# Kernel optimization log

Hardware: AMD Instinct MI355X
Metric: run time of the kernel (lower is better)

## Reference

```python
import jax, jax.numpy as jnp
import numpy as np

N, E, IN_C, HID, OUT_C, L = 100000, 1600000, 128, 128, 128, 3
BN_EPS = 1e-5


def setup_inputs() -> dict:
    key = jax.random.key(0)
    ks = jax.random.split(key, 16)
    inp = {
        "x": jax.random.normal(ks[0], (N, IN_C), dtype=jnp.float32),
        "edge_index": jax.random.randint(ks[1], (2, E), 0, N, dtype=jnp.int64),
        "edge_attr": jax.random.normal(ks[2], (E, 1), dtype=jnp.float32),
        # input/output projections (math uses [in, out] layout)
        "lin0_w": jax.random.normal(ks[3], (IN_C, HID), dtype=jnp.float32) / np.sqrt(IN_C),
        "lin0_b": jnp.zeros((HID,), dtype=jnp.float32),
        "lin1_w": jax.random.normal(ks[4], (HID, OUT_C), dtype=jnp.float32) / np.sqrt(HID),
        "lin1_b": jnp.zeros((OUT_C,), dtype=jnp.float32),
        # stacked GCNConv weights/biases
        "conv_w": jax.random.normal(ks[5], (L, HID, HID), dtype=jnp.float32) / np.sqrt(HID),
        "conv_b": jnp.zeros((L, HID), dtype=jnp.float32),
        # BatchNorm1d (eval mode: running stats are buffers)
        "bn_gamma": jnp.ones((L, HID), dtype=jnp.float32),
        "bn_beta": jnp.zeros((L, HID), dtype=jnp.float32),
        "bn_mean": 0.1 * jax.random.normal(ks[6], (L, HID), dtype=jnp.float32),
        "bn_var": jax.random.uniform(ks[7], (L, HID), minval=0.5, maxval=1.5, dtype=jnp.float32),
    }
    return inp


def reference(x, edge_index, edge_attr, lin0_w, lin0_b, lin1_w, lin1_b,
              conv_w, conv_b, bn_gamma, bn_beta, bn_mean, bn_var):
    n = x.shape[0]
    # GCN normalization with self-loops (computed once; identical every layer)
    loops = jnp.arange(n, dtype=edge_index.dtype)
    src = jnp.concatenate([edge_index[0], loops])  # [E+N]
    dst = jnp.concatenate([edge_index[1], loops])  # [E+N]
    deg = jax.ops.segment_sum(jnp.ones_like(src, dtype=x.dtype), dst, num_segments=n)
    dinv = jnp.where(deg > 0, deg ** -0.5, 0.0)
    norm = dinv[src] * dinv[dst]  # [E+N]

    # input projection + relu (dropout p used in eval -> identity)
    h = jax.nn.relu(x @ lin0_w + lin0_b)

    for l in range(L):
        hw = h @ conv_w[l]                                         # [N, H]
        msg = hw[src] * norm[:, None]                              # [E+N, H]
        agg = jax.ops.segment_sum(msg, dst, num_segments=n) + conv_b[l]
        # BatchNorm1d (inference) + ReLU activation
        h = (agg - bn_mean[l]) * jax.lax.rsqrt(bn_var[l] + BN_EPS) * bn_gamma[l] + bn_beta[l]
        h = jax.nn.relu(h)

    out = h @ lin1_w + lin1_b
    return out
```

## Files before the change

### kernel.cpp

```cpp
#include <hip/hip_runtime.h>
#include <hip/hip_fp16.h>


#define HIDC 128
#define BN_EPS 1e-5f
#define DPB 256
#define NBK 512
#define BIN_CHUNK 8192

typedef short bf16x8 __attribute__((ext_vector_type(8)));
typedef float f32x4 __attribute__((ext_vector_type(4)));

__device__ __forceinline__ unsigned short f2bf_rn(float x) {
    unsigned int u = __float_as_uint(x);
    unsigned int r = u + 0x7fffu + ((u >> 16) & 1u);
    return (unsigned short)(r >> 16);
}
__device__ __forceinline__ float bf2f(unsigned short b) {
    return __uint_as_float(((unsigned int)b) << 16);
}


__global__ void detect64(const unsigned int* ei, int* flag) {
    if (threadIdx.x != 0 || blockIdx.x != 0) return;
    int is64 = 1;
    for (int i = 0; i < 64; ++i) {
        if (ei[2 * i + 1] != 0u) { is64 = 0; break; }
    }
    *flag = is64;
}

__global__ __launch_bounds__(256) void bucket_count(const void* __restrict__ ei,
                                                    const int* __restrict__ flag,
                                                    int* __restrict__ bkt, int e) {
    __shared__ int h[NBK];
    int t = threadIdx.x;
    for (int i = t; i < NBK; i += 256) h[i] = 0;
    __syncthreads();
    int base = blockIdx.x * BIN_CHUNK;
    int cnt = e - base;
    if (cnt > BIN_CHUNK) cnt = BIN_CHUNK;
    if (*flag) {
        const long long* pd = (const long long*)ei + e;
        for (int i = t; i < cnt; i += 256) atomicAdd(&h[((int)pd[base + i]) >> 8], 1);
    } else {
        const int* pd = (const int*)ei + e;
        for (int i = t; i < cnt; i += 256) atomicAdd(&h[pd[base + i] >> 8], 1);
    }
    __syncthreads();
    for (int i = t; i < NBK; i += 256) if (h[i]) atomicAdd(&bkt[i], h[i]);
}

__global__ void scan_buckets(const int* __restrict__ bkt, int* __restrict__ bbase,
                             int* __restrict__ bc, int* __restrict__ rowptr,
                             int n, int e, int nbk) {
    __shared__ int s[NBK];
    int t = threadIdx.x;
    int v = (t < nbk) ? bkt[t] : 0;
    s[t] = v;
    __syncthreads();
    for (int off = 1; off < NBK; off <<= 1) {
        int val = (t >= off) ? s[t - off] : 0;
        __syncthreads();
        s[t] += val;
        __syncthreads();
    }
    int excl = s[t] - v;
    bbase[t] = excl;
    bc[t] = excl;
    if (t == 0) rowptr[n] = e;
}

__global__ __launch_bounds__(256) void bin_pairs(const void* __restrict__ ei,
                                                 const int* __restrict__ flag,
                                                 int* __restrict__ bc,
                                                 int2* __restrict__ staged, int e) {
    __shared__ int hist[NBK];
    __shared__ int lstart[NBK];
    __shared__ int gbase[NBK];
    __shared__ int sdata[256];
    __shared__ int2 stage[BIN_CHUNK];

    int t = threadIdx.x;
    int base = blockIdx.x * BIN_CHUNK;
    int cnt = e - base;
    if (cnt > BIN_CHUNK) cnt = BIN_CHUNK;
    int is64 = *flag;

    for (int i = t; i < NBK; i += 256) hist[i] = 0;
    __syncthreads();
    if (is64) {
        const long long* pd = (const long long*)ei + e;
        for (int i = t; i < cnt; i += 256) atomicAdd(&hist[((int)pd[base + i]) >> 8], 1);
    } else {
        const int* pd = (const int*)ei + e;
        for (int i = t; i < cnt; i += 256) atomicAdd(&hist[pd[base + i] >> 8], 1);
    }
    __syncthreads();

    int a0 = hist[2 * t], a1 = hist[2 * t + 1];
    int s = a0 + a1;
    sdata[t] = s;
    __syncthreads();
    for (int off = 1; off < 256; off <<= 1) {
        int val = (t >= off) ? sdata[t - off] : 0;
        __syncthreads();
        sdata[t] += val;
        __syncthreads();
    }
    int excl = sdata[t] - s;
    lstart[2 * t] = excl;
    lstart[2 * t + 1] = excl + a0;
    if (a0 > 0) gbase[2 * t] = atomicAdd(&bc[2 * t], a0);
    if (a1 > 0) gbase[2 * t + 1] = atomicAdd(&bc[2 * t + 1], a1);
    hist[2 * t] = excl;
    hist[2 * t + 1] = excl + a0;
    __syncthreads();

    if (is64) {
        const long long* ps = (const long long*)ei;
        const long long* pd = ps + e;
        for (int i = t; i < cnt; i += 256) {
            int2 p = make_int2((int)ps[base + i], (int)pd[base + i]);
            int pos = atomicAdd(&hist[p.y >> 8], 1);
            stage[pos] = p;
        }
    } else {
        const int* ps = (const int*)ei;
        const int* pd = ps + e;
        for (int i = t; i < cnt; i += 256) {
            int2 p = make_int2(ps[base + i], pd[base + i]);
            int pos = atomicAdd(&hist[p.y >> 8], 1);
            stage[pos] = p;
        }
    }
    __syncthreads();

    for (int i = t; i < cnt; i += 256) {
        int2 p = stage[i];
        int b = p.y >> 8;
        staged[gbase[b] + (i - lstart[b])] = p;
    }
}

__global__ __launch_bounds__(256) void fill_bucket(const int2* __restrict__ staged,
                                                   const int* __restrict__ bbase,
                                                   float* __restrict__ dinv,
                                                   int* __restrict__ rowptr,
                                                   int* __restrict__ col, int n) {
    __shared__ int cnt[DPB];
    __shared__ int scn[DPB];
    int b = blockIdx.x;
    int t = threadIdx.x;
    int dstart = b * DPB;
    int ebeg = bbase[b], eend = bbase[b + 1];
    cnt[t] = 0;
    __syncthreads();
    for (int i = ebeg + t; i < eend; i += 256)
        atomicAdd(&cnt[staged[i].y - dstart], 1);
    __syncthreads();
    int my = cnt[t];
    scn[t] = my;
    __syncthreads();
    for (int off = 1; off < 256; off <<= 1) {
        int val = (t >= off) ? scn[t - off] : 0;
        __syncthreads();
        scn[t] += val;
        __syncthreads();
    }
    int excl = scn[t] - my;
    int v = dstart + t;
    if (v < n) {
        rowptr[v] = ebeg + excl;
        dinv[v] = rsqrtf((float)(my + 1));
    }
    cnt[t] = excl;
    __syncthreads();
    for (int i = ebeg + t; i < eend; i += 256) {
        int2 p = staged[i];
        int pos = atomicAdd(&cnt[p.y - dstart], 1);
        col[ebeg + pos] = p.x;
    }
}


__global__ __launch_bounds__(256) void pack_w(const float* __restrict__ lin0,
                                              const float* __restrict__ conv,
                                              const float* __restrict__ lin1,
                                              uint4* __restrict__ wf) {
    int tid = blockIdx.x * 256 + threadIdx.x;
    if (tid >= 5 * 2048) return;
    int mat = tid >> 11;
    int rem = tid & 2047;
    int ks = rem >> 9;
    int tt = (rem >> 6) & 7;
    int l = rem & 63;
    const float* W = (mat == 0) ? lin0 : (mat == 4) ? lin1 : conv + (size_t)(mat - 1) * 16384;
    int kbase = ks * 32 + (l >> 4) * 8;
    int c = tt * 16 + (l & 15);
    unsigned int hi[4], lo[4];
#pragma unroll
    for (int d = 0; d < 4; ++d) {
        float w0 = W[(kbase + 2 * d) * 128 + c];
        float w1 = W[(kbase + 2 * d + 1) * 128 + c];
        unsigned short h0 = f2bf_rn(w0), h1 = f2bf_rn(w1);
        unsigned short l0 = f2bf_rn(w0 - bf2f(h0)), l1 = f2bf_rn(w1 - bf2f(h1));
        hi[d] = (unsigned int)h0 | ((unsigned int)h1 << 16);
        lo[d] = (unsigned int)l0 | ((unsigned int)l1 << 16);
    }
    int rec = (ks * 8 + tt) * 64 + l;
    wf[(size_t)mat * 4096 + rec] = make_uint4(hi[0], hi[1], hi[2], hi[3]);
    wf[(size_t)mat * 4096 + 2048 + rec] = make_uint4(lo[0], lo[1], lo[2], lo[3]);
}


template <int AFP16>
__global__ __launch_bounds__(512) void gemm_mfma(
    const void* __restrict__ A, const uint4* __restrict__ wf,
    const float* __restrict__ bias, const float* __restrict__ dinv,
    void* __restrict__ Cout, int M, int mode) {
    __shared__ uint4 WfL[4096];

    int t = threadIdx.x;
#pragma unroll
    for (int i = 0; i < 8; ++i) WfL[t + i * 512] = wf[t + i * 512];

    int wave = t >> 6, lane = t & 63;
    int lrow = lane & 15, lgrp = lane >> 4;
    int r0 = blockIdx.x * 128 + wave * 16;

    f32x4 acc[8];
#pragma unroll
    for (int i = 0; i < 8; ++i) acc[i] = (f32x4){0.f, 0.f, 0.f, 0.f};

    __syncthreads();

    int arow = r0 + lrow;
    if (arow >= M) arow = M - 1;
    const char* ap = (const char*)A +
        (AFP16 ? ((size_t)arow * 256 + lgrp * 16) : ((size_t)arow * 512 + lgrp * 32));

#pragma unroll
    for (int ks = 0; ks < 4; ++ks) {
        float av[8];
        if (AFP16) {
            uint4 q = *(const uint4*)(ap + ks * 64);
            unsigned int w[4] = {q.x, q.y, q.z, q.w};
#pragma unroll
            for (int d = 0; d < 4; ++d) {
                __half2 h2 = *(__half2*)&w[d];
                float2 f2 = __half22float2(h2);
                av[2 * d] = f2.x;
                av[2 * d + 1] = f2.y;
            }
        } else {
            float4 v0 = *(const float4*)(ap + ks * 128);
            float4 v1 = *(const float4*)(ap + ks * 128 + 16);
            av[0] = v0.x; av[1] = v0.y; av[2] = v0.z; av[3] = v0.w;
            av[4] = v1.x; av[5] = v1.y; av[6] = v1.z; av[7] = v1.w;
        }
        bf16x8 ahi, alo;
#pragma unroll
        for (int j = 0; j < 8; ++j) {
            unsigned short h = f2bf_rn(av[j]);
            ahi[j] = (short)h;
            alo[j] = (short)f2bf_rn(av[j] - bf2f(h));
        }
#pragma unroll
        for (int tt = 0; tt < 8; ++tt) {
            bf16x8 bhi = *(const bf16x8*)&WfL[(ks * 8 + tt) * 64 + lane];
            bf16x8 blo = *(const bf16x8*)&WfL[2048 + (ks * 8 + tt) * 64 + lane];
            acc[tt] = __builtin_amdgcn_mfma_f32_16x16x32_bf16(ahi, bhi, acc[tt], 0, 0, 0);
            acc[tt] = __builtin_amdgcn_mfma_f32_16x16x32_bf16(ahi, blo, acc[tt], 0, 0, 0);
            acc[tt] = __builtin_amdgcn_mfma_f32_16x16x32_bf16(alo, bhi, acc[tt], 0, 0, 0);
        }
    }

    int rbase = r0 + lgrp * 4;
    float dv[4] = {0.f, 0.f, 0.f, 0.f};
    if (mode == 1) {
#pragma unroll
        for (int j = 0; j < 4; ++j) dv[j] = (rbase + j < M) ? dinv[rbase + j] : 0.f;
    }
#pragma unroll
    for (int tt = 0; tt < 8; ++tt) {
        int c = tt * 16 + lrow;
        float bc_ = (mode != 1) ? bias[c] : 0.f;
#pragma unroll
        for (int j = 0; j < 4; ++j) {
            int r = rbase + j;
            if (r >= M) continue;
            float val = acc[tt][j];
            if (mode == 0) {
                ((__half*)Cout)[(size_t)r * 128 + c] = __float2half(fmaxf(val + bc_, 0.f));
            } else if (mode == 1) {
                ((__half*)Cout)[(size_t)r * 128 + c] = __float2half(val * dv[j]);
            } else {
                ((float*)Cout)[(size_t)r * 128 + c] = val + bc_;
            }
        }
    }
}


__global__ __launch_bounds__(256) void agg_bn_relu(
    const __half2* __restrict__ hw, const int* __restrict__ rowptr,
    const int* __restrict__ col, const float* __restrict__ dinv,
    const float* __restrict__ convb, const float* __restrict__ gamma,
    const float* __restrict__ beta, const float* __restrict__ mean,
    const float* __restrict__ var, __half2* __restrict__ hout, int n) {
    int lane = threadIdx.x & 63;
    int v = (blockIdx.x * 256 + threadIdx.x) >> 6;
    if (v >= n) return;

    float2 acc = __half22float2(hw[(size_t)v * 64 + lane]);

    int beg = rowptr[v], end = rowptr[v + 1];
    for (int p = beg; p < end; p += 64) {
        int cnt = end - p;
        if (cnt > 64) cnt = 64;
        int myc = (lane < cnt) ? col[p + lane] : 0;
        int j = 0;
        for (; j + 8 <= cnt; j += 8) {
            int u0 = __shfl(myc, j);
            int u1 = __shfl(myc, j + 1);
            int u2 = __shfl(myc, j + 2);
            int u3 = __shfl(myc, j + 3);
            int u4 = __shfl(myc, j + 4);
            int u5 = __shfl(myc, j + 5);
            int u6 = __shfl(myc, j + 6);
            int u7 = __shfl(myc, j + 7);
            float2 m0 = __half22float2(hw[(size_t)u0 * 64 + lane]);
            float2 m1 = __half22float2(hw[(size_t)u1 * 64 + lane]);
            float2 m2 = __half22float2(hw[(size_t)u2 * 64 + lane]);
            float2 m3 = __half22float2(hw[(size_t)u3 * 64 + lane]);
            float2 m4 = __half22float2(hw[(size_t)u4 * 64 + lane]);
            float2 m5 = __half22float2(hw[(size_t)u5 * 64 + lane]);
            float2 m6 = __half22float2(hw[(size_t)u6 * 64 + lane]);
            float2 m7 = __half22float2(hw[(size_t)u7 * 64 + lane]);
            acc.x += ((m0.x + m1.x) + (m2.x + m3.x)) + ((m4.x + m5.x) + (m6.x + m7.x));
            acc.y += ((m0.y + m1.y) + (m2.y + m3.y)) + ((m4.y + m5.y) + (m6.y + m7.y));
        }
        for (; j < cnt; ++j) {
            int u = __shfl(myc, j);
            float2 m = __half22float2(hw[(size_t)u * 64 + lane]);
            acc.x += m.x;
            acc.y += m.y;
        }
    }

    float dvv = dinv[v];
    int c0 = lane * 2;
    float2 g  = *(const float2*)(gamma + c0);
    float2 be = *(const float2*)(beta + c0);
    float2 mn = *(const float2*)(mean + c0);
    float2 va = *(const float2*)(var + c0);
    float2 cb = *(const float2*)(convb + c0);
    float s0 = g.x * rsqrtf(va.x + BN_EPS);
    float s1 = g.y * rsqrtf(va.y + BN_EPS);
    float o0 = (dvv * acc.x + cb.x - mn.x) * s0 + be.x;
    float o1 = (dvv * acc.y + cb.y - mn.y) * s1 + be.y;
    o0 = fmaxf(o0, 0.0f);
    o1 = fmaxf(o1, 0.0f);
    hout[(size_t)v * 64 + lane] = __floats2half2_rn(o0, o1);
}


extern "C" void kernel_launch(void* const* d_in, const int* in_sizes, int n_in,
                              void* d_out, int out_size, void* d_ws, size_t ws_size,
                              hipStream_t stream) {
    const float* x      = (const float*)d_in[0];
    const void*  ei     = d_in[1];
    const float* lin0_w = (const float*)d_in[3];
    const float* lin0_b = (const float*)d_in[4];
    const float* lin1_w = (const float*)d_in[5];
    const float* lin1_b = (const float*)d_in[6];
    const float* conv_w = (const float*)d_in[7];
    const float* conv_b = (const float*)d_in[8];
    const float* bn_g   = (const float*)d_in[9];
    const float* bn_b   = (const float*)d_in[10];
    const float* bn_m   = (const float*)d_in[11];
    const float* bn_v   = (const float*)d_in[12];

    int n = in_sizes[0] / HIDC;
    int e = in_sizes[1] / 2;
    int nbk = (n + DPB - 1) / DPB;

    char* ws = (char*)d_ws;
    size_t off = 0;
    auto alloc = [&](size_t bytes) -> void* {
        void* p = ws + off;
        off += (bytes + 255) & ~(size_t)255;
        return p;
    };
    __half2* h16    = (__half2*)alloc((size_t)n * HIDC * 2);
    __half2* hw     = (__half2*)alloc((size_t)n * HIDC * 2);
    int2*    staged = (int2*)alloc((size_t)e * 8);
    int*     col    = (int*)alloc((size_t)e * 4);
    float*   dinv   = (float*)alloc((size_t)n * 4);
    int*     rowptr = (int*)alloc(((size_t)n + 1) * 4);
    int*     bkt    = (int*)alloc((size_t)NBK * 4);
    int*     bbase  = (int*)alloc((size_t)(NBK + 1) * 4);
    int*     bc     = (int*)alloc((size_t)NBK * 4);
    uint4*   wf     = (uint4*)alloc((size_t)5 * 4096 * 16);
    int*     flag   = (int*)alloc(256);

    hipMemsetAsync(bkt, 0, (size_t)NBK * 4, stream);

    detect64<<<1, 64, 0, stream>>>((const unsigned int*)ei, flag);
    pack_w<<<40, 256, 0, stream>>>(lin0_w, conv_w, lin1_w, wf);

    int binb = (e + BIN_CHUNK - 1) / BIN_CHUNK;
    bucket_count<<<binb, 256, 0, stream>>>(ei, flag, bkt, e);
    scan_buckets<<<1, 512, 0, stream>>>(bkt, bbase, bc, rowptr, n, e, nbk);
    bin_pairs<<<binb, 256, 0, stream>>>(ei, flag, bc, staged, e);
    fill_bucket<<<nbk, 256, 0, stream>>>(staged, bbase, dinv, rowptr, col, n);

    int gb = (n + 127) / 128;
    gemm_mfma<0><<<gb, 512, 0, stream>>>(x, wf, lin0_b, nullptr, h16, n, 0);

    int ab = (n + 3) / 4;
    for (int l = 0; l < 3; ++l) {
        gemm_mfma<1><<<gb, 512, 0, stream>>>(h16, wf + (size_t)(1 + l) * 4096, nullptr, dinv, hw, n, 1);
        agg_bn_relu<<<ab, 256, 0, stream>>>(hw, rowptr, col, dinv,
                                            conv_b + (size_t)l * HIDC,
                                            bn_g + (size_t)l * HIDC, bn_b + (size_t)l * HIDC,
                                            bn_m + (size_t)l * HIDC, bn_v + (size_t)l * HIDC,
                                            h16, n);
    }
    gemm_mfma<1><<<gb, 512, 0, stream>>>(h16, wf + (size_t)4 * 4096, lin1_b, nullptr, d_out, n, 2);
}
```

Before: 382.7 us.

## Switch split-precision GEMM to fp16 MFMA and pack staged edge pairs into one int

The split-precision GEMM now uses fp16 MFMA instead of bf16. When the A input is already fp16 it is loaded straight into the operand with no conversion, and the low-part product is skipped, so those layers issue two MFMAs per tile instead of three. Edge staging packs the source index and the local destination offset into one 32-bit int, which halves the staged buffer traffic during CSR construction. The packing assumes node indices fit in 17 bits (N=100000 does). The fp16 hi/lo split has a narrower exponent range than bf16, so very large or very small weights or activations could lose accuracy.

```diff
diff --git a/kernel.cpp b/kernel.cpp
--- a/kernel.cpp
+++ b/kernel.cpp
@@ -8,17 +8,8 @@
 #define NBK 512
 #define BIN_CHUNK 8192
 
-typedef short bf16x8 __attribute__((ext_vector_type(8)));
+typedef _Float16 f16x8 __attribute__((ext_vector_type(8)));
 typedef float f32x4 __attribute__((ext_vector_type(4)));
-
-__device__ __forceinline__ unsigned short f2bf_rn(float x) {
-    unsigned int u = __float_as_uint(x);
-    unsigned int r = u + 0x7fffu + ((u >> 16) & 1u);
-    return (unsigned short)(r >> 16);
-}
-__device__ __forceinline__ float bf2f(unsigned short b) {
-    return __uint_as_float(((unsigned int)b) << 16);
-}
 
 
 __global__ void detect64(const unsigned int* ei, int* flag) {
@@ -74,7 +65,7 @@
 __global__ __launch_bounds__(256) void bin_pairs(const void* __restrict__ ei,
                                                  const int* __restrict__ flag,
                                                  int* __restrict__ bc,
-                                                 int2* __restrict__ staged, int e) {
+                                                 int* __restrict__ staged, int e) {
     __shared__ int hist[NBK];
     __shared__ int lstart[NBK];
     __shared__ int gbase[NBK];
@@ -139,11 +130,12 @@
     for (int i = t; i < cnt; i += 256) {
         int2 p = stage[i];
         int b = p.y >> 8;
-        staged[gbase[b] + (i - lstart[b])] = p;
-    }
-}
-
-__global__ __launch_bounds__(256) void fill_bucket(const int2* __restrict__ staged,
+        int packed = p.x | ((p.y & 255) << 17);
+        staged[gbase[b] + (i - lstart[b])] = packed;
+    }
+}
+
+__global__ __launch_bounds__(256) void fill_bucket(const int* __restrict__ staged,
                                                    const int* __restrict__ bbase,
                                                    float* __restrict__ dinv,
                                                    int* __restrict__ rowptr,
@@ -157,7 +149,7 @@
     cnt[t] = 0;
     __syncthreads();
     for (int i = ebeg + t; i < eend; i += 256)
-        atomicAdd(&cnt[staged[i].y - dstart], 1);
+        atomicAdd(&cnt[staged[i] >> 17], 1);
     __syncthreads();
     int my = cnt[t];
     scn[t] = my;
@@ -177,9 +169,9 @@
     cnt[t] = excl;
     __syncthreads();
     for (int i = ebeg + t; i < eend; i += 256) {
-        int2 p = staged[i];
-        int pos = atomicAdd(&cnt[p.y - dstart], 1);
-        col[ebeg + pos] = p.x;
+        int s = staged[i];
+        int pos = atomicAdd(&cnt[s >> 17], 1);
+        col[ebeg + pos] = s & 0x1FFFF;
     }
 }
 
@@ -203,10 +195,11 @@
     for (int d = 0; d < 4; ++d) {
         float w0 = W[(kbase + 2 * d) * 128 + c];
         float w1 = W[(kbase + 2 * d + 1) * 128 + c];
-        unsigned short h0 = f2bf_rn(w0), h1 = f2bf_rn(w1);
-        unsigned short l0 = f2bf_rn(w0 - bf2f(h0)), l1 = f2bf_rn(w1 - bf2f(h1));
-        hi[d] = (unsigned int)h0 | ((unsigned int)h1 << 16);
-        lo[d] = (unsigned int)l0 | ((unsigned int)l1 << 16);
+        __half h0 = __float2half_rn(w0), h1 = __float2half_rn(w1);
+        __half l0 = __float2half_rn(w0 - __half2float(h0));
+        __half l1 = __float2half_rn(w1 - __half2float(h1));
+        hi[d] = (unsigned int)__half_as_ushort(h0) | ((unsigned int)__half_as_ushort(h1) << 16);
+        lo[d] = (unsigned int)__half_as_ushort(l0) | ((unsigned int)__half_as_ushort(l1) << 16);
     }
     int rec = (ks * 8 + tt) * 64 + l;
     wf[(size_t)mat * 4096 + rec] = make_uint4(hi[0], hi[1], hi[2], hi[3]);
@@ -242,37 +235,28 @@
 
 #pragma unroll
     for (int ks = 0; ks < 4; ++ks) {
-        float av[8];
+        f16x8 ahi, alo;
         if (AFP16) {
-            uint4 q = *(const uint4*)(ap + ks * 64);
-            unsigned int w[4] = {q.x, q.y, q.z, q.w};
-#pragma unroll
-            for (int d = 0; d < 4; ++d) {
-                __half2 h2 = *(__half2*)&w[d];
-                float2 f2 = __half22float2(h2);
-                av[2 * d] = f2.x;
-                av[2 * d + 1] = f2.y;
-            }
+            ahi = *(const f16x8*)(ap + ks * 64);
         } else {
             float4 v0 = *(const float4*)(ap + ks * 128);
             float4 v1 = *(const float4*)(ap + ks * 128 + 16);
-            av[0] = v0.x; av[1] = v0.y; av[2] = v0.z; av[3] = v0.w;
-            av[4] = v1.x; av[5] = v1.y; av[6] = v1.z; av[7] = v1.w;
-        }
-        bf16x8 ahi, alo;
-#pragma unroll
-        for (int j = 0; j < 8; ++j) {
-            unsigned short h = f2bf_rn(av[j]);
-            ahi[j] = (short)h;
-            alo[j] = (short)f2bf_rn(av[j] - bf2f(h));
+            float av[8] = {v0.x, v0.y, v0.z, v0.w, v1.x, v1.y, v1.z, v1.w};
+#pragma unroll
+            for (int j = 0; j < 8; ++j) {
+                _Float16 h = (_Float16)av[j];
+                ahi[j] = h;
+                alo[j] = (_Float16)(av[j] - (float)h);
+            }
         }
 #pragma unroll
         for (int tt = 0; tt < 8; ++tt) {
-            bf16x8 bhi = *(const bf16x8*)&WfL[(ks * 8 + tt) * 64 + lane];
-            bf16x8 blo = *(const bf16x8*)&WfL[2048 + (ks * 8 + tt) * 64 + lane];
-            acc[tt] = __builtin_amdgcn_mfma_f32_16x16x32_bf16(ahi, bhi, acc[tt], 0, 0, 0);
-            acc[tt] = __builtin_amdgcn_mfma_f32_16x16x32_bf16(ahi, blo, acc[tt], 0, 0, 0);
-            acc[tt] = __builtin_amdgcn_mfma_f32_16x16x32_bf16(alo, bhi, acc[tt], 0, 0, 0);
+            f16x8 bhi = *(const f16x8*)&WfL[(ks * 8 + tt) * 64 + lane];
+            f16x8 blo = *(const f16x8*)&WfL[2048 + (ks * 8 + tt) * 64 + lane];
+            acc[tt] = __builtin_amdgcn_mfma_f32_16x16x32_f16(ahi, bhi, acc[tt], 0, 0, 0);
+            acc[tt] = __builtin_amdgcn_mfma_f32_16x16x32_f16(ahi, blo, acc[tt], 0, 0, 0);
+            if (!AFP16)
+                acc[tt] = __builtin_amdgcn_mfma_f32_16x16x32_f16(alo, bhi, acc[tt], 0, 0, 0);
         }
     }
 
@@ -395,7 +379,7 @@
     };
     __half2* h16    = (__half2*)alloc((size_t)n * HIDC * 2);
     __half2* hw     = (__half2*)alloc((size_t)n * HIDC * 2);
-    int2*    staged = (int2*)alloc((size_t)e * 8);
+    int*     staged = (int*)alloc((size_t)e * 4);
     int*     col    = (int*)alloc((size_t)e * 4);
     float*   dinv   = (float*)alloc((size_t)n * 4);
     int*     rowptr = (int*)alloc(((size_t)n + 1) * 4);
```

Result: faster. 369.5 us (-3.4%).
